# Kernel optimization log

Hardware: AMD Instinct MI355X
Metric: run time of the kernel (lower is better)

The kernel has to match this reference:

```python
import jax, jax.numpy as jnp
import numpy as np

B, N, K, C_IN, C_OUT = 8, 24576, 16, 64, 64
BN_EPS = 1e-5


def setup_inputs() -> dict:
    key = jax.random.key(0)
    k1, k2, k3, k4, k5 = jax.random.split(key, 5)
    x = jax.random.normal(k1, (B, N, C_IN), dtype=jnp.float32)
    W = jax.random.normal(k2, (C_OUT, C_IN), dtype=jnp.float32) * 0.05  # Linear weight (no bias)
    # BN affine params; module inits gamma to `init` (0.0) but that zeroes the output,
    # so we use a perturbed gamma for a meaningful correctness baseline.
    gamma = 1.0 + 0.1 * jax.random.normal(k3, (C_OUT,), dtype=jnp.float32)
    beta = 0.1 * jax.random.normal(k4, (C_OUT,), dtype=jnp.float32)
    knn = jax.random.randint(k5, (B, N, K), 0, N, dtype=jnp.int32)
    return {"x": x, "W": W, "gamma": gamma, "beta": beta, "knn": knn}


def _vector_feature(h, knn):
    # h: [B, N, C], knn: [B, N, K] -> max over neighbors of (h_j - h_i): [B, N, C]
    b, n, k = knn.shape
    nbr = jnp.take_along_axis(h, knn.reshape(b, n * k, 1), axis=1).reshape(b, n, k, -1)
    return jnp.max(nbr - h[:, :, None, :], axis=2)


def reference(x, W, gamma, beta, knn):
    h = jnp.einsum('bnc,oc->bno', x, W)            # linear, no bias
    v = _vector_feature(h, knn)                    # knn edge max-pool
    # BatchNorm1d in training mode: batch stats over B*N rows, per channel
    mean = jnp.mean(v, axis=(0, 1))
    var = jnp.mean(jnp.square(v - mean), axis=(0, 1))  # biased variance
    out = (v - mean) * jax.lax.rsqrt(var + BN_EPS) * gamma + beta
    return out
```

## Files before the change

kernel.cpp:

```cpp
#include <hip/hip_runtime.h>
#include <hip/hip_bf16.h>

typedef short s16x8 __attribute__((ext_vector_type(8)));
typedef float f32x4 __attribute__((ext_vector_type(4)));
typedef unsigned short u16x8 __attribute__((ext_vector_type(8)));

static constexpr int Bc   = 8;
static constexpr int Nn   = 24576;
static constexpr int Kk   = 16;
static constexpr int Cc   = 64;
static constexpr int Rr   = Bc * Nn;
static constexpr float EPS = 1e-5f;

__device__ __forceinline__ unsigned short f2bf(float f) {
    union { float f; unsigned int u; } c; c.f = f;
    unsigned int r = c.u + 0x7FFFu + ((c.u >> 16) & 1u);
    return (unsigned short)(r >> 16);
}
__device__ __forceinline__ float bf2f(unsigned short u) {
    union { unsigned int u; float f; } c; c.u = ((unsigned int)u) << 16; return c.f;
}

__global__ __launch_bounds__(256) void linear_mfma_kernel(
    const float* __restrict__ x, const float* __restrict__ W,
    __hip_bfloat16* __restrict__ h)
{
    const int tid  = threadIdx.x;
    const int l    = tid & 63;
    const int wave = tid >> 6;
    const int batch = blockIdx.x & 7;
    const int qb    = blockIdx.x >> 3;
    const int wib   = qb * 4 + wave;

    const int lr = l & 15;
    const int kg = (l >> 4) * 8;
    const int dr = (l >> 4) * 4;

    s16x8 bfrag[4][2];
#pragma unroll
    for (int ct = 0; ct < 4; ++ct)
#pragma unroll
        for (int kc = 0; kc < 2; ++kc) {
            const float* bp = W + (ct * 16 + lr) * 64 + kc * 32 + kg;
            f32x4 b0 = *reinterpret_cast<const f32x4*>(bp);
            f32x4 b1 = *reinterpret_cast<const f32x4*>(bp + 4);
            s16x8 f;
            f[0] = (short)f2bf(b0[0]); f[1] = (short)f2bf(b0[1]);
            f[2] = (short)f2bf(b0[2]); f[3] = (short)f2bf(b0[3]);
            f[4] = (short)f2bf(b1[0]); f[5] = (short)f2bf(b1[1]);
            f[6] = (short)f2bf(b1[2]); f[7] = (short)f2bf(b1[3]);
            bfrag[ct][kc] = f;
        }

    unsigned short* hu = (unsigned short*)h;
    const int tiles_per_batch = Nn / 16;
    for (int t = wib; t < tiles_per_batch; t += 1024) {
        const int row0 = batch * Nn + t * 16;
        const float* ap = x + (size_t)(row0 + lr) * 64 + kg;
        f32x4 a0 = *reinterpret_cast<const f32x4*>(ap);
        f32x4 a1 = *reinterpret_cast<const f32x4*>(ap + 4);
        f32x4 a2 = *reinterpret_cast<const f32x4*>(ap + 32);
        f32x4 a3 = *reinterpret_cast<const f32x4*>(ap + 36);
        s16x8 fa0, fa1;
        fa0[0] = (short)f2bf(a0[0]); fa0[1] = (short)f2bf(a0[1]);
        fa0[2] = (short)f2bf(a0[2]); fa0[3] = (short)f2bf(a0[3]);
        fa0[4] = (short)f2bf(a1[0]); fa0[5] = (short)f2bf(a1[1]);
        fa0[6] = (short)f2bf(a1[2]); fa0[7] = (short)f2bf(a1[3]);
        fa1[0] = (short)f2bf(a2[0]); fa1[1] = (short)f2bf(a2[1]);
        fa1[2] = (short)f2bf(a2[2]); fa1[3] = (short)f2bf(a2[3]);
        fa1[4] = (short)f2bf(a3[0]); fa1[5] = (short)f2bf(a3[1]);
        fa1[6] = (short)f2bf(a3[2]); fa1[7] = (short)f2bf(a3[3]);

        f32x4 acc[4];
#pragma unroll
        for (int ct = 0; ct < 4; ++ct) { acc[ct] = (f32x4){0.f, 0.f, 0.f, 0.f}; }
#pragma unroll
        for (int ct = 0; ct < 4; ++ct) {
            acc[ct] = __builtin_amdgcn_mfma_f32_16x16x32_bf16(fa0, bfrag[ct][0], acc[ct], 0, 0, 0);
            acc[ct] = __builtin_amdgcn_mfma_f32_16x16x32_bf16(fa1, bfrag[ct][1], acc[ct], 0, 0, 0);
        }
#pragma unroll
        for (int ct = 0; ct < 4; ++ct)
#pragma unroll
            for (int r = 0; r < 4; ++r)
                hu[(size_t)(row0 + dr + r) * 64 + ct * 16 + lr] = f2bf(acc[ct][r]);
    }
}

__global__ __launch_bounds__(256) void gather_bn_kernel(
    const __hip_bfloat16* __restrict__ h, const int* __restrict__ knn,
    __hip_bfloat16* __restrict__ v, float* __restrict__ stats)
{
    const int tid   = threadIdx.x;
    const int lane  = tid & 63;
    const int wave  = tid >> 6;
    const int batch = blockIdx.x & 7;
    const int qb    = blockIdx.x >> 3;
    const int wib   = qb * 4 + wave;

    const unsigned short* hu = (const unsigned short*)h;
    unsigned short* vu = (unsigned short*)v;
    const int bbase = batch * Nn;

    float lsum = 0.f, lsq = 0.f;

    for (int r = wib * 2; r < Nn; r += 2048) {
        const int row0 = bbase + r, row1 = row0 + 1;
        const int i0 = knn[(size_t)row0 * Kk + (lane & 15)];
        const int i1 = knn[(size_t)row1 * Kk + (lane & 15)];
        const float o0 = bf2f(hu[(size_t)row0 * 64 + lane]);
        const float o1 = bf2f(hu[(size_t)row1 * 64 + lane]);
        float m0 = -3e38f, m1 = -3e38f;
#pragma unroll
        for (int k = 0; k < Kk; ++k) {
            const int j0 = __shfl(i0, k);
            const int j1 = __shfl(i1, k);
            const float g0 = bf2f(hu[(size_t)(bbase + j0) * 64 + lane]);
            const float g1 = bf2f(hu[(size_t)(bbase + j1) * 64 + lane]);
            m0 = fmaxf(m0, g0);
            m1 = fmaxf(m1, g1);
        }
        const float v0 = m0 - o0, v1 = m1 - o1;
        vu[(size_t)row0 * 64 + lane] = f2bf(v0);
        vu[(size_t)row1 * 64 + lane] = f2bf(v1);
        lsum += v0 + v1;
        lsq  += v0 * v0 + v1 * v1;
    }

    __shared__ float s_sum[4][64];
    __shared__ float s_sq[4][64];
    s_sum[wave][lane] = lsum;
    s_sq[wave][lane]  = lsq;
    __syncthreads();
    if (wave == 0) {
        const float a = s_sum[0][lane] + s_sum[1][lane] + s_sum[2][lane] + s_sum[3][lane];
        const float q = s_sq[0][lane]  + s_sq[1][lane]  + s_sq[2][lane]  + s_sq[3][lane];
        atomicAdd(&stats[lane], a);
        atomicAdd(&stats[64 + lane], q);
    }
}

__global__ __launch_bounds__(64) void finalize_stats_kernel(
    const float* __restrict__ stats, const float* __restrict__ gamma,
    const float* __restrict__ beta, float* __restrict__ ss)
{
    const int o = threadIdx.x;
    const float inv_count = 1.0f / (float)Rr;
    const float mean = stats[o] * inv_count;
    const float var  = stats[64 + o] * inv_count - mean * mean;
    const float sc   = gamma[o] * rsqrtf(var + EPS);
    ss[o]      = sc;
    ss[64 + o] = beta[o] - mean * sc;
}

__global__ __launch_bounds__(256) void norm_kernel(
    const __hip_bfloat16* __restrict__ v, const float* __restrict__ ss,
    float* __restrict__ out)
{
    __shared__ float sc[64], sh[64];
    if (threadIdx.x < 64) {
        sc[threadIdx.x] = ss[threadIdx.x];
        sh[threadIdx.x] = ss[64 + threadIdx.x];
    }
    __syncthreads();

    const int batch = blockIdx.x & 7;
    const int qb    = blockIdx.x >> 3;
    const u16x8* vu = (const u16x8*)v;
    const int per_batch8 = Nn * 64 / 8;
    const size_t base8 = (size_t)batch * per_batch8;

    for (int li = qb * 256 + threadIdx.x; li < per_batch8; li += 256 * 256) {
        const size_t i = base8 + li;
        u16x8 t = vu[i];
        const int c = (li * 8) & 63;
        f32x4 r0, r1;
        r0[0] = bf2f(t[0]) * sc[c + 0] + sh[c + 0];
        r0[1] = bf2f(t[1]) * sc[c + 1] + sh[c + 1];
        r0[2] = bf2f(t[2]) * sc[c + 2] + sh[c + 2];
        r0[3] = bf2f(t[3]) * sc[c + 3] + sh[c + 3];
        r1[0] = bf2f(t[4]) * sc[c + 4] + sh[c + 4];
        r1[1] = bf2f(t[5]) * sc[c + 5] + sh[c + 5];
        r1[2] = bf2f(t[6]) * sc[c + 6] + sh[c + 6];
        r1[3] = bf2f(t[7]) * sc[c + 7] + sh[c + 7];
        f32x4* op = reinterpret_cast<f32x4*>(out + i * 8);
        __builtin_nontemporal_store(r0, op);
        __builtin_nontemporal_store(r1, op + 1);
    }
}

extern "C" void kernel_launch(void* const* d_in, const int* in_sizes, int n_in,
                              void* d_out, int out_size, void* d_ws, size_t ws_size,
                              hipStream_t stream)
{
    const float* x     = (const float*)d_in[0];
    const float* W     = (const float*)d_in[1];
    const float* gamma = (const float*)d_in[2];
    const float* beta  = (const float*)d_in[3];
    const int*   knn   = (const int*)d_in[4];
    float*       out   = (float*)d_out;

    __hip_bfloat16* h = (__hip_bfloat16*)d_ws;
    __hip_bfloat16* v = h + (size_t)Rr * 64;
    float* stats = (float*)((char*)d_ws + 2 * (size_t)Rr * 64 * sizeof(__hip_bfloat16));
    float* ss    = stats + 128;

    (void)hipMemsetAsync(stats, 0, 128 * sizeof(float), stream);

    linear_mfma_kernel<<<2048, 256, 0, stream>>>(x, W, h);
    gather_bn_kernel<<<2048, 256, 0, stream>>>(h, knn, v, stats);
    finalize_stats_kernel<<<1, 64, 0, stream>>>(stats, gamma, beta, ss);
    norm_kernel<<<2048, 256, 0, stream>>>(v, ss, out);
}
```

Measured before the change: 221.8 us.

## Widen gather to 32-bit bf16 pairs and fold stat setup into neighbouring kernels

The gather kernel now has each lane load a packed pair of bf16 channels as one 32-bit word, so half a wave covers a 64-channel row and each wave handles four rows per iteration instead of two. This halves the number of gather load instructions per row, at the cost of an extra cross-half shuffle when reducing the statistics. The memset is replaced by zeroing inside the linear kernel, and the finalize kernel is folded into the norm kernel's prologue, removing two launches. Every norm block now recomputes the per-channel scale and shift, which is a small amount of redundant work.

```diff
diff --git a/kernel.cpp b/kernel.cpp
--- a/kernel.cpp
+++ b/kernel.cpp
@@ -20,11 +20,22 @@
 __device__ __forceinline__ float bf2f(unsigned short u) {
     union { unsigned int u; float f; } c; c.u = ((unsigned int)u) << 16; return c.f;
 }
+__device__ __forceinline__ float bflo(unsigned g) {
+    union { unsigned u; float f; } c; c.u = g << 16; return c.f;
+}
+__device__ __forceinline__ float bfhi(unsigned g) {
+    union { unsigned u; float f; } c; c.u = g & 0xffff0000u; return c.f;
+}
+__device__ __forceinline__ unsigned packbf(float lo, float hi) {
+    return (unsigned)f2bf(lo) | ((unsigned)f2bf(hi) << 16);
+}
 
 __global__ __launch_bounds__(256) void linear_mfma_kernel(
     const float* __restrict__ x, const float* __restrict__ W,
-    __hip_bfloat16* __restrict__ h)
-{
+    __hip_bfloat16* __restrict__ h, float* __restrict__ stats)
+{
+    if (blockIdx.x == 0 && threadIdx.x < 128) stats[threadIdx.x] = 0.f;
+
     const int tid  = threadIdx.x;
     const int l    = tid & 63;
     const int wave = tid >> 6;
@@ -92,75 +103,83 @@
     __hip_bfloat16* __restrict__ v, float* __restrict__ stats)
 {
     const int tid   = threadIdx.x;
-    const int lane  = tid & 63;
+    const int l     = tid & 63;
     const int wave  = tid >> 6;
     const int batch = blockIdx.x & 7;
     const int qb    = blockIdx.x >> 3;
     const int wib   = qb * 4 + wave;
 
-    const unsigned short* hu = (const unsigned short*)h;
-    unsigned short* vu = (unsigned short*)v;
+    const unsigned* hu32 = (const unsigned*)h;
+    unsigned* vu32 = (unsigned*)v;
     const int bbase = batch * Nn;
 
-    float lsum = 0.f, lsq = 0.f;
-
-    for (int r = wib * 2; r < Nn; r += 2048) {
-        const int row0 = bbase + r, row1 = row0 + 1;
-        const int i0 = knn[(size_t)row0 * Kk + (lane & 15)];
-        const int i1 = knn[(size_t)row1 * Kk + (lane & 15)];
-        const float o0 = bf2f(hu[(size_t)row0 * 64 + lane]);
-        const float o1 = bf2f(hu[(size_t)row1 * 64 + lane]);
-        float m0 = -3e38f, m1 = -3e38f;
+    const int half = l >> 5;
+    const int c2   = l & 31;
+    const int kl   = l & 15;
+
+    float sum_lo = 0.f, sum_hi = 0.f, sq_lo = 0.f, sq_hi = 0.f;
+
+    for (int r = wib * 4; r < Nn; r += 4096) {
+        const int rowA = bbase + r + half;
+        const int rowC = bbase + r + 2 + half;
+        const int ia = knn[(size_t)rowA * Kk + kl];
+        const int ic = knn[(size_t)rowC * Kk + kl];
+        const unsigned oa = hu32[(size_t)rowA * 32 + c2];
+        const unsigned oc = hu32[(size_t)rowC * 32 + c2];
+        float mAlo = -3e38f, mAhi = -3e38f, mClo = -3e38f, mChi = -3e38f;
 #pragma unroll
         for (int k = 0; k < Kk; ++k) {
-            const int j0 = __shfl(i0, k);
-            const int j1 = __shfl(i1, k);
-            const float g0 = bf2f(hu[(size_t)(bbase + j0) * 64 + lane]);
-            const float g1 = bf2f(hu[(size_t)(bbase + j1) * 64 + lane]);
-            m0 = fmaxf(m0, g0);
-            m1 = fmaxf(m1, g1);
+            const int ja = __shfl(ia, (l & 32) + k);
+            const int jc = __shfl(ic, (l & 32) + k);
+            const unsigned ga = hu32[(size_t)(bbase + ja) * 32 + c2];
+            const unsigned gc = hu32[(size_t)(bbase + jc) * 32 + c2];
+            mAlo = fmaxf(mAlo, bflo(ga)); mAhi = fmaxf(mAhi, bfhi(ga));
+            mClo = fmaxf(mClo, bflo(gc)); mChi = fmaxf(mChi, bfhi(gc));
         }
-        const float v0 = m0 - o0, v1 = m1 - o1;
-        vu[(size_t)row0 * 64 + lane] = f2bf(v0);
-        vu[(size_t)row1 * 64 + lane] = f2bf(v1);
-        lsum += v0 + v1;
-        lsq  += v0 * v0 + v1 * v1;
-    }
-
-    __shared__ float s_sum[4][64];
-    __shared__ float s_sq[4][64];
-    s_sum[wave][lane] = lsum;
-    s_sq[wave][lane]  = lsq;
+        const float vAlo = mAlo - bflo(oa), vAhi = mAhi - bfhi(oa);
+        const float vClo = mClo - bflo(oc), vChi = mChi - bfhi(oc);
+        vu32[(size_t)rowA * 32 + c2] = packbf(vAlo, vAhi);
+        vu32[(size_t)rowC * 32 + c2] = packbf(vClo, vChi);
+        sum_lo += vAlo + vClo; sum_hi += vAhi + vChi;
+        sq_lo  += vAlo * vAlo + vClo * vClo;
+        sq_hi  += vAhi * vAhi + vChi * vChi;
+    }
+
+    sum_lo += __shfl_xor(sum_lo, 32); sum_hi += __shfl_xor(sum_hi, 32);
+    sq_lo  += __shfl_xor(sq_lo, 32);  sq_hi  += __shfl_xor(sq_hi, 32);
+
+    __shared__ float s[4][4][32];
+    if (half == 0) {
+        s[0][wave][c2] = sum_lo; s[1][wave][c2] = sum_hi;
+        s[2][wave][c2] = sq_lo;  s[3][wave][c2] = sq_hi;
+    }
     __syncthreads();
-    if (wave == 0) {
-        const float a = s_sum[0][lane] + s_sum[1][lane] + s_sum[2][lane] + s_sum[3][lane];
-        const float q = s_sq[0][lane]  + s_sq[1][lane]  + s_sq[2][lane]  + s_sq[3][lane];
-        atomicAdd(&stats[lane], a);
-        atomicAdd(&stats[64 + lane], q);
-    }
-}
-
-__global__ __launch_bounds__(64) void finalize_stats_kernel(
-    const float* __restrict__ stats, const float* __restrict__ gamma,
-    const float* __restrict__ beta, float* __restrict__ ss)
-{
-    const int o = threadIdx.x;
-    const float inv_count = 1.0f / (float)Rr;
-    const float mean = stats[o] * inv_count;
-    const float var  = stats[64 + o] * inv_count - mean * mean;
-    const float sc   = gamma[o] * rsqrtf(var + EPS);
-    ss[o]      = sc;
-    ss[64 + o] = beta[o] - mean * sc;
+    if (wave == 0 && half == 0) {
+        const float a0 = s[0][0][c2] + s[0][1][c2] + s[0][2][c2] + s[0][3][c2];
+        const float a1 = s[1][0][c2] + s[1][1][c2] + s[1][2][c2] + s[1][3][c2];
+        const float q0 = s[2][0][c2] + s[2][1][c2] + s[2][2][c2] + s[2][3][c2];
+        const float q1 = s[3][0][c2] + s[3][1][c2] + s[3][2][c2] + s[3][3][c2];
+        atomicAdd(&stats[2 * c2],      a0);
+        atomicAdd(&stats[2 * c2 + 1],  a1);
+        atomicAdd(&stats[64 + 2 * c2], q0);
+        atomicAdd(&stats[64 + 2 * c2 + 1], q1);
+    }
 }
 
 __global__ __launch_bounds__(256) void norm_kernel(
-    const __hip_bfloat16* __restrict__ v, const float* __restrict__ ss,
+    const __hip_bfloat16* __restrict__ v, const float* __restrict__ stats,
+    const float* __restrict__ gamma, const float* __restrict__ beta,
     float* __restrict__ out)
 {
     __shared__ float sc[64], sh[64];
     if (threadIdx.x < 64) {
-        sc[threadIdx.x] = ss[threadIdx.x];
-        sh[threadIdx.x] = ss[64 + threadIdx.x];
+        const int o = threadIdx.x;
+        const float inv = 1.0f / (float)Rr;
+        const float mean = stats[o] * inv;
+        const float var  = stats[64 + o] * inv - mean * mean;
+        const float s    = gamma[o] * rsqrtf(var + EPS);
+        sc[o] = s;
+        sh[o] = beta[o] - mean * s;
     }
     __syncthreads();
 
@@ -203,12 +222,8 @@
     __hip_bfloat16* h = (__hip_bfloat16*)d_ws;
     __hip_bfloat16* v = h + (size_t)Rr * 64;
     float* stats = (float*)((char*)d_ws + 2 * (size_t)Rr * 64 * sizeof(__hip_bfloat16));
-    float* ss    = stats + 128;
-
-    (void)hipMemsetAsync(stats, 0, 128 * sizeof(float), stream);
-
-    linear_mfma_kernel<<<2048, 256, 0, stream>>>(x, W, h);
+
+    linear_mfma_kernel<<<2048, 256, 0, stream>>>(x, W, h, stats);
     gather_bn_kernel<<<2048, 256, 0, stream>>>(h, knn, v, stats);
-    finalize_stats_kernel<<<1, 64, 0, stream>>>(stats, gamma, beta, ss);
-    norm_kernel<<<2048, 256, 0, stream>>>(v, ss, out);
-}
+    norm_kernel<<<2048, 256, 0, stream>>>(v, stats, gamma, beta, out);
+}
```

After: 253.6 us. 1.14x slower.

## Prefetch knn rows in gather with 3-row ILP and fold BN finalize into norm

Applied to the files above, without the earlier changes.

The gather kernel now handles three rows per iteration with a fixed trip count. It software-prefetches the next iteration's neighbour indices and center values, so more gather loads are in flight. The memset and the separate finalize kernel are removed: stats are zeroed by block 0 of the linear kernel, and each norm block recomputes scale and shift. This cuts two launches, at the cost of more registers and redundant per-block finalize work.

```diff
diff --git a/kernel.cpp b/kernel.cpp
--- a/kernel.cpp
+++ b/kernel.cpp
@@ -23,8 +23,10 @@
 
 __global__ __launch_bounds__(256) void linear_mfma_kernel(
     const float* __restrict__ x, const float* __restrict__ W,
-    __hip_bfloat16* __restrict__ h)
-{
+    __hip_bfloat16* __restrict__ h, float* __restrict__ stats)
+{
+    if (blockIdx.x == 0 && threadIdx.x < 128) stats[threadIdx.x] = 0.f;
+
     const int tid  = threadIdx.x;
     const int l    = tid & 63;
     const int wave = tid >> 6;
@@ -101,30 +103,53 @@
     const unsigned short* hu = (const unsigned short*)h;
     unsigned short* vu = (unsigned short*)v;
     const int bbase = batch * Nn;
+    const int kl    = lane & 15;
 
     float lsum = 0.f, lsq = 0.f;
 
-    for (int r = wib * 2; r < Nn; r += 2048) {
-        const int row0 = bbase + r, row1 = row0 + 1;
-        const int i0 = knn[(size_t)row0 * Kk + (lane & 15)];
-        const int i1 = knn[(size_t)row1 * Kk + (lane & 15)];
-        const float o0 = bf2f(hu[(size_t)row0 * 64 + lane]);
-        const float o1 = bf2f(hu[(size_t)row1 * 64 + lane]);
-        float m0 = -3e38f, m1 = -3e38f;
+    int r = wib * 3;
+    int i0 = knn[(size_t)(bbase + r + 0) * Kk + kl];
+    int i1 = knn[(size_t)(bbase + r + 1) * Kk + kl];
+    int i2 = knn[(size_t)(bbase + r + 2) * Kk + kl];
+    unsigned short o0 = hu[(size_t)(bbase + r + 0) * 64 + lane];
+    unsigned short o1 = hu[(size_t)(bbase + r + 1) * 64 + lane];
+    unsigned short o2 = hu[(size_t)(bbase + r + 2) * 64 + lane];
+
+    for (int it = 0; it < 8; ++it) {
+        const int rn = r + 3072;
+        int ni0 = 0, ni1 = 0, ni2 = 0;
+        unsigned short no0 = 0, no1 = 0, no2 = 0;
+        if (it < 7) {
+            ni0 = knn[(size_t)(bbase + rn + 0) * Kk + kl];
+            ni1 = knn[(size_t)(bbase + rn + 1) * Kk + kl];
+            ni2 = knn[(size_t)(bbase + rn + 2) * Kk + kl];
+            no0 = hu[(size_t)(bbase + rn + 0) * 64 + lane];
+            no1 = hu[(size_t)(bbase + rn + 1) * 64 + lane];
+            no2 = hu[(size_t)(bbase + rn + 2) * 64 + lane];
+        }
+
+        float m0 = -3e38f, m1 = -3e38f, m2 = -3e38f;
 #pragma unroll
         for (int k = 0; k < Kk; ++k) {
             const int j0 = __shfl(i0, k);
             const int j1 = __shfl(i1, k);
-            const float g0 = bf2f(hu[(size_t)(bbase + j0) * 64 + lane]);
-            const float g1 = bf2f(hu[(size_t)(bbase + j1) * 64 + lane]);
-            m0 = fmaxf(m0, g0);
-            m1 = fmaxf(m1, g1);
-        }
-        const float v0 = m0 - o0, v1 = m1 - o1;
-        vu[(size_t)row0 * 64 + lane] = f2bf(v0);
-        vu[(size_t)row1 * 64 + lane] = f2bf(v1);
-        lsum += v0 + v1;
-        lsq  += v0 * v0 + v1 * v1;
+            const int j2 = __shfl(i2, k);
+            m0 = fmaxf(m0, bf2f(hu[(size_t)(bbase + j0) * 64 + lane]));
+            m1 = fmaxf(m1, bf2f(hu[(size_t)(bbase + j1) * 64 + lane]));
+            m2 = fmaxf(m2, bf2f(hu[(size_t)(bbase + j2) * 64 + lane]));
+        }
+        const float v0 = m0 - bf2f(o0);
+        const float v1 = m1 - bf2f(o1);
+        const float v2 = m2 - bf2f(o2);
+        vu[(size_t)(bbase + r + 0) * 64 + lane] = f2bf(v0);
+        vu[(size_t)(bbase + r + 1) * 64 + lane] = f2bf(v1);
+        vu[(size_t)(bbase + r + 2) * 64 + lane] = f2bf(v2);
+        lsum += v0 + v1 + v2;
+        lsq  += v0 * v0 + v1 * v1 + v2 * v2;
+
+        r = rn;
+        i0 = ni0; i1 = ni1; i2 = ni2;
+        o0 = no0; o1 = no1; o2 = no2;
     }
 
     __shared__ float s_sum[4][64];
@@ -140,27 +165,20 @@
     }
 }
 
-__global__ __launch_bounds__(64) void finalize_stats_kernel(
-    const float* __restrict__ stats, const float* __restrict__ gamma,
-    const float* __restrict__ beta, float* __restrict__ ss)
-{
-    const int o = threadIdx.x;
-    const float inv_count = 1.0f / (float)Rr;
-    const float mean = stats[o] * inv_count;
-    const float var  = stats[64 + o] * inv_count - mean * mean;
-    const float sc   = gamma[o] * rsqrtf(var + EPS);
-    ss[o]      = sc;
-    ss[64 + o] = beta[o] - mean * sc;
-}
-
 __global__ __launch_bounds__(256) void norm_kernel(
-    const __hip_bfloat16* __restrict__ v, const float* __restrict__ ss,
+    const __hip_bfloat16* __restrict__ v, const float* __restrict__ stats,
+    const float* __restrict__ gamma, const float* __restrict__ beta,
     float* __restrict__ out)
 {
     __shared__ float sc[64], sh[64];
     if (threadIdx.x < 64) {
-        sc[threadIdx.x] = ss[threadIdx.x];
-        sh[threadIdx.x] = ss[64 + threadIdx.x];
+        const int o = threadIdx.x;
+        const float inv = 1.0f / (float)Rr;
+        const float mean = stats[o] * inv;
+        const float var  = stats[64 + o] * inv - mean * mean;
+        const float s    = gamma[o] * rsqrtf(var + EPS);
+        sc[o] = s;
+        sh[o] = beta[o] - mean * s;
     }
     __syncthreads();
 
@@ -203,12 +221,8 @@
     __hip_bfloat16* h = (__hip_bfloat16*)d_ws;
     __hip_bfloat16* v = h + (size_t)Rr * 64;
     float* stats = (float*)((char*)d_ws + 2 * (size_t)Rr * 64 * sizeof(__hip_bfloat16));
-    float* ss    = stats + 128;
-
-    (void)hipMemsetAsync(stats, 0, 128 * sizeof(float), stream);
-
-    linear_mfma_kernel<<<2048, 256, 0, stream>>>(x, W, h);
+
+    linear_mfma_kernel<<<2048, 256, 0, stream>>>(x, W, h, stats);
     gather_bn_kernel<<<2048, 256, 0, stream>>>(h, knn, v, stats);
-    finalize_stats_kernel<<<1, 64, 0, stream>>>(stats, gamma, beta, ss);
-    norm_kernel<<<2048, 256, 0, stream>>>(v, ss, out);
-}
+    norm_kernel<<<2048, 256, 0, stream>>>(v, stats, gamma, beta, out);
+}
```

Measured after the change: 269.0 us. 21.3% more time.
